# Kernel tuning notes

Hardware: AMD Instinct MI355X
Metric: run time of the kernel (lower is better)

## Reference

```python
import jax, jax.numpy as jnp
import numpy as np

NEG_SLOPE = 0.2


def gat_conv(x, edge_index, W, a_src, a_dst, b, concat):
    """PyG-style GATConv: add self-loops, linear, edge attention, scatter-softmax, scatter-add."""
    N = x.shape[0]
    H, C = a_src.shape
    loop = jnp.arange(N)
    src = jnp.concatenate([edge_index[0], loop])  # source j (messages flow j -> i)
    dst = jnp.concatenate([edge_index[1], loop])  # target i (aggregation node)
    h = (x @ W).reshape(N, H, C)                  # [N,H,C]
    alpha_s = jnp.sum(h * a_src, axis=-1)         # [N,H]
    alpha_d = jnp.sum(h * a_dst, axis=-1)         # [N,H]
    e = jax.nn.leaky_relu(alpha_s[src] + alpha_d[dst], NEG_SLOPE)  # [E,H]
    # numerically stable scatter-softmax over edges grouped by destination node
    m = jax.ops.segment_max(e, dst, num_segments=N)                # [N,H]
    ex = jnp.exp(e - m[dst])
    denom = jax.ops.segment_sum(ex, dst, num_segments=N)           # [N,H]
    alpha = ex / (denom[dst] + 1e-16)                              # [E,H]
    out = jax.ops.segment_sum(h[src] * alpha[:, :, None], dst, num_segments=N)  # [N,H,C]
    out = out.reshape(N, H * C) if concat else out.mean(axis=1)
    return out + b


def setup_inputs() -> dict:
    key = jax.random.key(0)
    ks = jax.random.split(key, 12)
    N, E, F_IN, HID, OUT, HEADS = 100000, 1600000, 128, 128, 64, 4
    C1 = HID // HEADS
    x = jax.random.normal(ks[0], (N, F_IN), dtype=jnp.float32)
    edge_index = jax.random.randint(ks[1], (2, E), 0, N, dtype=jnp.int64)
    s = 0.05
    return {
        "x": x,
        "edge_index": edge_index,
        "W1": jax.random.normal(ks[2], (F_IN, HEADS * C1), dtype=jnp.float32) * s,
        "a_src1": jax.random.normal(ks[3], (HEADS, C1), dtype=jnp.float32) * s,
        "a_dst1": jax.random.normal(ks[4], (HEADS, C1), dtype=jnp.float32) * s,
        "b1": jnp.zeros((HEADS * C1,), dtype=jnp.float32),
        "W2": jax.random.normal(ks[5], (HID, OUT), dtype=jnp.float32) * s,
        "a_src2": jax.random.normal(ks[6], (1, OUT), dtype=jnp.float32) * s,
        "a_dst2": jax.random.normal(ks[7], (1, OUT), dtype=jnp.float32) * s,
        "b2": jnp.zeros((OUT,), dtype=jnp.float32),
    }


def reference(x, edge_index, W1, a_src1, a_dst1, b1, W2, a_src2, a_dst2, b2):
    h = jax.nn.elu(gat_conv(x, edge_index, W1, a_src1, a_dst1, b1, concat=True))
    # F.dropout(p=0.5, training=False) is the identity in eval mode
    out = gat_conv(h, edge_index, W2, a_src2, a_dst2, b2, concat=False)
    return out
```

## Files before the change

kernel.cpp:

```cpp
#include <hip/hip_runtime.h>
#include <hip/hip_fp16.h>
#include <math.h>
#include <string.h>


#define BSH 9
#define DPB 512
#define NBK 256
#define CH1 16384
#define LOG2E 1.44269504088896f

__device__ __forceinline__ float exp2_fast(float x) {
#if __has_builtin(__builtin_amdgcn_exp2f)
    return __builtin_amdgcn_exp2f(x);
#else
    return exp2f(x);
#endif
}


__global__ __launch_bounds__(256) void bucket_hist(const int* __restrict__ ei, int E, int N,
                                                   unsigned* __restrict__ bcount) {
    __shared__ unsigned hist[NBK];
    int t = threadIdx.x;
    hist[t] = 0;
    __syncthreads();
    int Etot = E + N;
    for (int k = blockIdx.x * 256 + t; k < Etot; k += gridDim.x * 256) {
        int d = (k < E) ? ei[E + k] : (k - E);
        atomicAdd(&hist[d >> BSH], 1u);
    }
    __syncthreads();
    unsigned c = hist[t];
    if (c) atomicAdd(&bcount[t], c);
}

__global__ void scan_buckets(const unsigned* __restrict__ bcount, unsigned* __restrict__ bbase,
                             unsigned* __restrict__ bcursor) {
    __shared__ unsigned s[NBK];
    int t = threadIdx.x;
    unsigned v = bcount[t];
    s[t] = v;
    __syncthreads();
    for (int o = 1; o < NBK; o <<= 1) {
        unsigned add = (t >= o) ? s[t - o] : 0;
        __syncthreads();
        s[t] += add;
        __syncthreads();
    }
    unsigned excl = s[t] - v;
    bbase[t] = excl;
    bcursor[t] = excl;
    if (t == NBK - 1) bbase[NBK] = excl + v;
}

__global__ __launch_bounds__(256) void bucket_scatter(const int* __restrict__ ei, int E, int N,
                                                      unsigned* __restrict__ bcursor,
                                                      uint2* __restrict__ rec) {
    __shared__ unsigned hist[NBK];
    __shared__ unsigned base[NBK];
    int t = threadIdx.x;
    hist[t] = 0;
    __syncthreads();
    int Etot = E + N;
    int k0 = blockIdx.x * CH1;
    int k1 = min(k0 + CH1, Etot);
    for (int k = k0 + t; k < k1; k += 256) {
        int d = (k < E) ? ei[E + k] : (k - E);
        atomicAdd(&hist[d >> BSH], 1u);
    }
    __syncthreads();
    unsigned c = hist[t];
    base[t] = c ? atomicAdd(&bcursor[t], c) : 0u;
    hist[t] = 0;
    __syncthreads();
    for (int k = k0 + t; k < k1; k += 256) {
        int s, d;
        if (k < E) { s = ei[k]; d = ei[E + k]; } else { s = d = k - E; }
        int b = d >> BSH;
        unsigned r = atomicAdd(&hist[b], 1u);
        rec[base[b] + r] = make_uint2((unsigned)s, (unsigned)d);
    }
}

__global__ __launch_bounds__(256) void bucket_sort(const uint2* __restrict__ rec,
                                                   const unsigned* __restrict__ bbase,
                                                   int* __restrict__ offs, int* __restrict__ srcs,
                                                   int N, int Etot) {
    __shared__ unsigned hist[DPB];
    __shared__ unsigned tsum[256];
    int t = threadIdx.x, bb = blockIdx.x;
    unsigned r0 = bbase[bb], r1 = bbase[bb + 1];
    hist[t] = 0;
    hist[t + 256] = 0;
    __syncthreads();
    int dlo = bb << BSH;
    for (unsigned k = r0 + t; k < r1; k += 256) {
        uint2 e = rec[k];
        atomicAdd(&hist[e.y - dlo], 1u);
    }
    __syncthreads();
    unsigned h0 = hist[2 * t], h1 = hist[2 * t + 1];
    tsum[t] = h0 + h1;
    __syncthreads();
    for (int o = 1; o < 256; o <<= 1) {
        unsigned a = (t >= o) ? tsum[t - o] : 0;
        __syncthreads();
        tsum[t] += a;
        __syncthreads();
    }
    unsigned tb = tsum[t] - (h0 + h1);
    int d0 = dlo + 2 * t;
    if (d0 < N) offs[d0] = (int)(r0 + tb);
    if (d0 + 1 < N) offs[d0 + 1] = (int)(r0 + tb + h0);
    hist[2 * t] = tb;
    hist[2 * t + 1] = tb + h0;
    __syncthreads();
    for (unsigned k = r0 + t; k < r1; k += 256) {
        uint2 e = rec[k];
        unsigned r = atomicAdd(&hist[e.y - dlo], 1u);
        srcs[r0 + r] = (int)e.x;
    }
    if (bb == 0 && t == 0) offs[N] = Etot;
}


template <int NC, int H, typename InT, typename OutT>
__global__ __launch_bounds__(256) void gemm_k128(const InT* __restrict__ A,
                                                 const float* __restrict__ B,
                                                 OutT* __restrict__ C,
                                                 const float* __restrict__ a_src,
                                                 const float* __restrict__ a_dst,
                                                 float* __restrict__ as,
                                                 float* __restrict__ ad, int M) {
    constexpr int BM = 64, BK = 32, K = 128;
    constexpr int TPR = NC / 4;
    constexpr int R = BM / (256 / TPR);
    constexpr int TXH = TPR / H;
    __shared__ float AsT[BK][BM + 4];
    __shared__ float Bs[BK][NC];
    int tid = threadIdx.x;
    int tx = tid % TPR, ty = tid / TPR;
    int rowBase = blockIdx.x * BM;
    float acc[R][4] = {};
    for (int k0 = 0; k0 < K; k0 += BK) {
#pragma unroll
        for (int i = 0; i < 4; ++i) {
            int lin = tid + i * 256;
            int row = lin >> 4;
            int kp = lin & 15;
            int grow = rowBase + row;
            if (grow >= M) grow = M - 1;
            float2 v;
            if constexpr (sizeof(InT) == 2) {
                __half2 hv = *reinterpret_cast<const __half2*>((const __half*)A + (size_t)grow * K + k0 + kp * 2);
                v = __half22float2(hv);
            } else {
                v = *reinterpret_cast<const float2*>((const float*)A + (size_t)grow * K + k0 + kp * 2);
            }
            AsT[kp * 2][row] = v.x;
            AsT[kp * 2 + 1][row] = v.y;
        }
#pragma unroll
        for (int i = 0; i < (BK * NC) / 1024; ++i) {
            int lin = tid + i * 256;
            int row = lin / (NC / 4);
            int col4 = lin % (NC / 4);
            float4 v = *reinterpret_cast<const float4*>(B + (size_t)(k0 + row) * NC + col4 * 4);
            *reinterpret_cast<float4*>(&Bs[row][col4 * 4]) = v;
        }
        __syncthreads();
#pragma unroll
        for (int kk = 0; kk < BK; ++kk) {
            float4 bv = *reinterpret_cast<const float4*>(&Bs[kk][tx * 4]);
            float a[R];
#pragma unroll
            for (int r4 = 0; r4 < R; r4 += 4) {
                float4 av = *reinterpret_cast<const float4*>(&AsT[kk][ty * R + r4]);
                a[r4] = av.x; a[r4 + 1] = av.y; a[r4 + 2] = av.z; a[r4 + 3] = av.w;
            }
#pragma unroll
            for (int r = 0; r < R; ++r) {
                acc[r][0] = fmaf(a[r], bv.x, acc[r][0]);
                acc[r][1] = fmaf(a[r], bv.y, acc[r][1]);
                acc[r][2] = fmaf(a[r], bv.z, acc[r][2]);
                acc[r][3] = fmaf(a[r], bv.w, acc[r][3]);
            }
        }
        __syncthreads();
    }
    float4 asv = *reinterpret_cast<const float4*>(a_src + tx * 4);
    float4 adv = *reinterpret_cast<const float4*>(a_dst + tx * 4);
#pragma unroll
    for (int r = 0; r < R; ++r) {
        int grow = rowBase + ty * R + r;
        bool live = grow < M;
        if (live) {
            if constexpr (sizeof(OutT) == 2) {
                __half2 p0 = __floats2half2_rn(acc[r][0], acc[r][1]);
                __half2 p1 = __floats2half2_rn(acc[r][2], acc[r][3]);
                __half2* cp = reinterpret_cast<__half2*>((__half*)C + (size_t)grow * NC + tx * 4);
                cp[0] = p0;
                cp[1] = p1;
            } else {
                float4 v = make_float4(acc[r][0], acc[r][1], acc[r][2], acc[r][3]);
                *reinterpret_cast<float4*>((float*)C + (size_t)grow * NC + tx * 4) = v;
            }
        }
        float ps = acc[r][0] * asv.x + acc[r][1] * asv.y + acc[r][2] * asv.z + acc[r][3] * asv.w;
        float pd = acc[r][0] * adv.x + acc[r][1] * adv.y + acc[r][2] * adv.z + acc[r][3] * adv.w;
#pragma unroll
        for (int o = 1; o < TXH; o <<= 1) {
            ps += __shfl_xor(ps, o, 64);
            pd += __shfl_xor(pd, o, 64);
        }
        if ((tx & (TXH - 1)) == 0 && live) {
            int head = tx / TXH;
            as[(size_t)grow * H + head] = ps * LOG2E;
            ad[(size_t)grow * H + head] = pd * LOG2E;
        }
    }
}


template <int H, int F, bool DOELU, typename OutT>
__global__ __launch_bounds__(256) void aggregateQ(const __half* __restrict__ h,
                                                  const float* __restrict__ as,
                                                  const float* __restrict__ ad,
                                                  const int* __restrict__ offs,
                                                  const int* __restrict__ srcs,
                                                  const float* __restrict__ bias,
                                                  OutT* __restrict__ out, int N) {
    constexpr int CPL = F / 16;
    constexpr int NH2 = CPL / 2;
    unsigned wave = (blockIdx.x * blockDim.x + threadIdx.x) >> 6;
    unsigned lane = threadIdx.x & 63;
    unsigned lig = lane & 15;
    unsigned node = wave * 4u + (lane >> 4);
    bool live = node < (unsigned)N;
    unsigned nc = live ? node : (unsigned)(N - 1);
    unsigned head = (lig * CPL) / (F / H);
    float adv = ad[nc * H + head];
    int e0 = offs[nc], e1 = offs[nc + 1];
    int deg = e1 - e0, e1m1 = e1 - 1;
    int md = deg;
    md = max(md, __shfl_xor(md, 16, 64));
    md = max(md, __shfl_xor(md, 32, 64));
    float2 acc[NH2] = {};
    float den = 0.f;
    for (int k = 0; k < md; k += 2) {
        unsigned ja = (unsigned)srcs[min(e0 + k, e1m1)];
        unsigned jb = (unsigned)srcs[min(e0 + k + 1, e1m1)];
        float ta = as[ja * H + head] + adv;
        float tb = as[jb * H + head] + adv;
        __half2 ha[NH2], hb[NH2];
        if constexpr (NH2 == 4) {
            uint4 va = *reinterpret_cast<const uint4*>(h + ja * (unsigned)F + lig * CPL);
            uint4 vb = *reinterpret_cast<const uint4*>(h + jb * (unsigned)F + lig * CPL);
            memcpy(ha, &va, 16);
            memcpy(hb, &vb, 16);
        } else {
            uint2 va = *reinterpret_cast<const uint2*>(h + ja * (unsigned)F + lig * CPL);
            uint2 vb = *reinterpret_cast<const uint2*>(h + jb * (unsigned)F + lig * CPL);
            memcpy(ha, &va, 8);
            memcpy(hb, &vb, 8);
        }
        float xa = exp2_fast(fmaxf(ta, 0.2f * ta));
        float xb = exp2_fast(fmaxf(tb, 0.2f * tb));
        xa = (k < deg) ? xa : 0.f;
        xb = (k + 1 < deg) ? xb : 0.f;
#pragma unroll
        for (int q = 0; q < NH2; ++q) {
            float2 fa = __half22float2(ha[q]);
            float2 fb = __half22float2(hb[q]);
            acc[q].x = fmaf(xa, fa.x, acc[q].x);
            acc[q].y = fmaf(xa, fa.y, acc[q].y);
            acc[q].x = fmaf(xb, fb.x, acc[q].x);
            acc[q].y = fmaf(xb, fb.y, acc[q].y);
        }
        den += xa + xb;
    }
    float r = 1.0f / (den + 1e-16f);
    if (!live) return;
    const float* bp = bias + lig * CPL;
    if constexpr (sizeof(OutT) == 2) {
        __half2 st[NH2];
#pragma unroll
        for (int q = 0; q < NH2; ++q) {
            float v0 = acc[q].x * r + bp[2 * q];
            float v1 = acc[q].y * r + bp[2 * q + 1];
            if constexpr (DOELU) {
                v0 = (v0 > 0.f) ? v0 : expm1f(v0);
                v1 = (v1 > 0.f) ? v1 : expm1f(v1);
            }
            st[q] = __floats2half2_rn(v0, v1);
        }
        if constexpr (NH2 == 4) {
            uint4 v; memcpy(&v, st, 16);
            *reinterpret_cast<uint4*>((__half*)out + node * (unsigned)F + lig * CPL) = v;
        } else {
            uint2 v; memcpy(&v, st, 8);
            *reinterpret_cast<uint2*>((__half*)out + node * (unsigned)F + lig * CPL) = v;
        }
    } else {
        float vs[CPL];
#pragma unroll
        for (int q = 0; q < NH2; ++q) {
            float v0 = acc[q].x * r + bp[2 * q];
            float v1 = acc[q].y * r + bp[2 * q + 1];
            if constexpr (DOELU) {
                v0 = (v0 > 0.f) ? v0 : expm1f(v0);
                v1 = (v1 > 0.f) ? v1 : expm1f(v1);
            }
            vs[2 * q] = v0;
            vs[2 * q + 1] = v1;
        }
#pragma unroll
        for (int q4 = 0; q4 < CPL; q4 += 4) {
            float4 v = make_float4(vs[q4], vs[q4 + 1], vs[q4 + 2], vs[q4 + 3]);
            *reinterpret_cast<float4*>((float*)out + node * (unsigned)F + lig * CPL + q4) = v;
        }
    }
}


extern "C" void kernel_launch(void* const* d_in, const int* in_sizes, int n_in,
                              void* d_out, int out_size, void* d_ws, size_t ws_size,
                              hipStream_t stream) {
    const float* x      = (const float*)d_in[0];
    const int*   ei     = (const int*)d_in[1];
    const float* W1     = (const float*)d_in[2];
    const float* a_src1 = (const float*)d_in[3];
    const float* a_dst1 = (const float*)d_in[4];
    const float* b1     = (const float*)d_in[5];
    const float* W2     = (const float*)d_in[6];
    const float* a_src2 = (const float*)d_in[7];
    const float* a_dst2 = (const float*)d_in[8];
    const float* b2     = (const float*)d_in[9];
    float* out = (float*)d_out;

    const int N = out_size / 64;
    const int E = in_sizes[1] / 2;
    const int Etot = E + N;

    size_t off = 0;
    auto carve = [&](size_t bytes) -> void* {
        void* p = (char*)d_ws + off;
        off += (bytes + 255) & ~(size_t)255;
        return p;
    };
    __half* h1      = (__half*)carve((size_t)N * 128 * 2);
    __half* hmid    = (__half*)carve((size_t)N * 128 * 2);
    float* as1      = (float*)carve((size_t)N * 4 * 4);
    float* ad1      = (float*)carve((size_t)N * 4 * 4);
    float* as2      = (float*)carve((size_t)N * 4);
    float* ad2      = (float*)carve((size_t)N * 4);
    int*   offs     = (int*)carve((size_t)(N + 1) * 4);
    int*   srcs     = (int*)carve((size_t)Etot * 4);
    uint2* rec      = (uint2*)carve((size_t)Etot * 8);
    unsigned* bcount  = (unsigned*)carve(NBK * 4);
    unsigned* bbase   = (unsigned*)carve((NBK + 1) * 4);
    unsigned* bcursor = (unsigned*)carve(NBK * 4);
    __half* h2      = h1;

    hipMemsetAsync(bcount, 0, NBK * sizeof(unsigned), stream);
    bucket_hist<<<128, 256, 0, stream>>>(ei, E, N, bcount);
    scan_buckets<<<1, 256, 0, stream>>>(bcount, bbase, bcursor);
    bucket_scatter<<<(Etot + CH1 - 1) / CH1, 256, 0, stream>>>(ei, E, N, bcursor, rec);
    bucket_sort<<<(N + DPB - 1) / DPB, 256, 0, stream>>>(rec, bbase, offs, srcs, N, Etot);

    gemm_k128<128, 4, float, __half><<<(N + 63) / 64, 256, 0, stream>>>(
        x, W1, h1, a_src1, a_dst1, as1, ad1, N);
    aggregateQ<4, 128, true, __half><<<(N + 15) / 16, 256, 0, stream>>>(
        h1, as1, ad1, offs, srcs, b1, hmid, N);

    gemm_k128<64, 1, __half, __half><<<(N + 63) / 64, 256, 0, stream>>>(
        hmid, W2, h2, a_src2, a_dst2, as2, ad2, N);
    aggregateQ<1, 64, false, float><<<(N + 15) / 16, 256, 0, stream>>>(
        h2, as2, ad2, offs, srcs, b2, out, N);
}
```

Measured before the change: 390.0 us.

## Pack sort records into 32 bits and split layer-1 aggregation into channel halves

Bucket records now pack the source index (17 bits) and the destination offset within its bucket into one 32-bit word instead of a uint2, which halves record traffic in scatter and sort. The layer-1 aggregation is split into two launches, each covering 64 of the 128 channels. This shrinks the per-launch gather working set so it has a better chance of staying in cache, but the edge lists, attention scores and exponentials are computed twice. The packing assumes N fits in 17 bits (up to 131072 nodes).

After: 416.0 us. 6.7% more time.

```diff
diff --git a/kernel.cpp b/kernel.cpp
--- a/kernel.cpp
+++ b/kernel.cpp
@@ -56,7 +56,7 @@
 
 __global__ __launch_bounds__(256) void bucket_scatter(const int* __restrict__ ei, int E, int N,
                                                       unsigned* __restrict__ bcursor,
-                                                      uint2* __restrict__ rec) {
+                                                      unsigned* __restrict__ rec) {
     __shared__ unsigned hist[NBK];
     __shared__ unsigned base[NBK];
     int t = threadIdx.x;
@@ -79,11 +79,11 @@
         if (k < E) { s = ei[k]; d = ei[E + k]; } else { s = d = k - E; }
         int b = d >> BSH;
         unsigned r = atomicAdd(&hist[b], 1u);
-        rec[base[b] + r] = make_uint2((unsigned)s, (unsigned)d);
-    }
-}
-
-__global__ __launch_bounds__(256) void bucket_sort(const uint2* __restrict__ rec,
+        rec[base[b] + r] = (unsigned)s | ((unsigned)(d & (DPB - 1)) << 17);
+    }
+}
+
+__global__ __launch_bounds__(256) void bucket_sort(const unsigned* __restrict__ rec,
                                                    const unsigned* __restrict__ bbase,
                                                    int* __restrict__ offs, int* __restrict__ srcs,
                                                    int N, int Etot) {
@@ -96,8 +96,8 @@
     __syncthreads();
     int dlo = bb << BSH;
     for (unsigned k = r0 + t; k < r1; k += 256) {
-        uint2 e = rec[k];
-        atomicAdd(&hist[e.y - dlo], 1u);
+        unsigned e = rec[k];
+        atomicAdd(&hist[e >> 17], 1u);
     }
     __syncthreads();
     unsigned h0 = hist[2 * t], h1 = hist[2 * t + 1];
@@ -117,9 +117,9 @@
     hist[2 * t + 1] = tb + h0;
     __syncthreads();
     for (unsigned k = r0 + t; k < r1; k += 256) {
-        uint2 e = rec[k];
-        unsigned r = atomicAdd(&hist[e.y - dlo], 1u);
-        srcs[r0 + r] = (int)e.x;
+        unsigned e = rec[k];
+        unsigned r = atomicAdd(&hist[e >> 17], 1u);
+        srcs[r0 + r] = (int)(e & 0x1FFFFu);
     }
     if (bb == 0 && t == 0) offs[N] = Etot;
 }
@@ -223,7 +223,7 @@
 }
 
 
-template <int H, int F, bool DOELU, typename OutT>
+template <int H, int ROWS, int COFF, int CW, bool DOELU, typename OutT>
 __global__ __launch_bounds__(256) void aggregateQ(const __half* __restrict__ h,
                                                   const float* __restrict__ as,
                                                   const float* __restrict__ ad,
@@ -231,7 +231,7 @@
                                                   const int* __restrict__ srcs,
                                                   const float* __restrict__ bias,
                                                   OutT* __restrict__ out, int N) {
-    constexpr int CPL = F / 16;
+    constexpr int CPL = CW / 16;
     constexpr int NH2 = CPL / 2;
     unsigned wave = (blockIdx.x * blockDim.x + threadIdx.x) >> 6;
     unsigned lane = threadIdx.x & 63;
@@ -239,7 +239,8 @@
     unsigned node = wave * 4u + (lane >> 4);
     bool live = node < (unsigned)N;
     unsigned nc = live ? node : (unsigned)(N - 1);
-    unsigned head = (lig * CPL) / (F / H);
+    unsigned chan = COFF + lig * CPL;
+    unsigned head = (chan * H) / ROWS;
     float adv = ad[nc * H + head];
     int e0 = offs[nc], e1 = offs[nc + 1];
     int deg = e1 - e0, e1m1 = e1 - 1;
@@ -255,13 +256,13 @@
         float tb = as[jb * H + head] + adv;
         __half2 ha[NH2], hb[NH2];
         if constexpr (NH2 == 4) {
-            uint4 va = *reinterpret_cast<const uint4*>(h + ja * (unsigned)F + lig * CPL);
-            uint4 vb = *reinterpret_cast<const uint4*>(h + jb * (unsigned)F + lig * CPL);
+            uint4 va = *reinterpret_cast<const uint4*>(h + ja * (unsigned)ROWS + chan);
+            uint4 vb = *reinterpret_cast<const uint4*>(h + jb * (unsigned)ROWS + chan);
             memcpy(ha, &va, 16);
             memcpy(hb, &vb, 16);
         } else {
-            uint2 va = *reinterpret_cast<const uint2*>(h + ja * (unsigned)F + lig * CPL);
-            uint2 vb = *reinterpret_cast<const uint2*>(h + jb * (unsigned)F + lig * CPL);
+            uint2 va = *reinterpret_cast<const uint2*>(h + ja * (unsigned)ROWS + chan);
+            uint2 vb = *reinterpret_cast<const uint2*>(h + jb * (unsigned)ROWS + chan);
             memcpy(ha, &va, 8);
             memcpy(hb, &vb, 8);
         }
@@ -282,7 +283,7 @@
     }
     float r = 1.0f / (den + 1e-16f);
     if (!live) return;
-    const float* bp = bias + lig * CPL;
+    const float* bp = bias + chan;
     if constexpr (sizeof(OutT) == 2) {
         __half2 st[NH2];
 #pragma unroll
@@ -297,10 +298,10 @@
         }
         if constexpr (NH2 == 4) {
             uint4 v; memcpy(&v, st, 16);
-            *reinterpret_cast<uint4*>((__half*)out + node * (unsigned)F + lig * CPL) = v;
+            *reinterpret_cast<uint4*>((__half*)out + node * (unsigned)ROWS + chan) = v;
         } else {
             uint2 v; memcpy(&v, st, 8);
-            *reinterpret_cast<uint2*>((__half*)out + node * (unsigned)F + lig * CPL) = v;
+            *reinterpret_cast<uint2*>((__half*)out + node * (unsigned)ROWS + chan) = v;
         }
     } else {
         float vs[CPL];
@@ -318,7 +319,7 @@
 #pragma unroll
         for (int q4 = 0; q4 < CPL; q4 += 4) {
             float4 v = make_float4(vs[q4], vs[q4 + 1], vs[q4 + 2], vs[q4 + 3]);
-            *reinterpret_cast<float4*>((float*)out + node * (unsigned)F + lig * CPL + q4) = v;
+            *reinterpret_cast<float4*>((float*)out + node * (unsigned)ROWS + chan + q4) = v;
         }
     }
 }
@@ -357,7 +358,7 @@
     float* ad2      = (float*)carve((size_t)N * 4);
     int*   offs     = (int*)carve((size_t)(N + 1) * 4);
     int*   srcs     = (int*)carve((size_t)Etot * 4);
-    uint2* rec      = (uint2*)carve((size_t)Etot * 8);
+    unsigned* rec   = (unsigned*)carve((size_t)Etot * 4);
     unsigned* bcount  = (unsigned*)carve(NBK * 4);
     unsigned* bbase   = (unsigned*)carve((NBK + 1) * 4);
     unsigned* bcursor = (unsigned*)carve(NBK * 4);
@@ -371,11 +372,13 @@
 
     gemm_k128<128, 4, float, __half><<<(N + 63) / 64, 256, 0, stream>>>(
         x, W1, h1, a_src1, a_dst1, as1, ad1, N);
-    aggregateQ<4, 128, true, __half><<<(N + 15) / 16, 256, 0, stream>>>(
+    aggregateQ<4, 128, 0, 64, true, __half><<<(N + 15) / 16, 256, 0, stream>>>(
+        h1, as1, ad1, offs, srcs, b1, hmid, N);
+    aggregateQ<4, 128, 64, 64, true, __half><<<(N + 15) / 16, 256, 0, stream>>>(
         h1, as1, ad1, offs, srcs, b1, hmid, N);
 
     gemm_k128<64, 1, __half, __half><<<(N + 63) / 64, 256, 0, stream>>>(
         hmid, W2, h2, a_src2, a_dst2, as2, ad2, N);
-    aggregateQ<1, 64, false, float><<<(N + 15) / 16, 256, 0, stream>>>(
+    aggregateQ<1, 64, 0, 64, false, float><<<(N + 15) / 16, 256, 0, stream>>>(
         h2, as2, ad2, offs, srcs, b2, out, N);
 }
```
